# Optimization experiments

Measured on AMD Instinct MI355X. Metric: run time of the kernel, lower is better.

## Reference

```python
import jax, jax.numpy as jnp
import numpy as np

N = 1048576            # batch of query points
D = 3                  # n_in
N_LEVELS = 16
F_PER_LEVEL = 2
LOG2_T = 19
T = 1 << LOG2_T        # hash table size per level
MIN_RES = 16
MAX_RES = 512

# instant-NGP spatial hash primes (first prime = 1)
_PRIMES = np.array([1, 2654435761, 805459861], dtype=np.uint32)
# 2^D corner offsets of the interpolation cell, [8, D]
_OFFSETS = np.stack(np.meshgrid(*([np.arange(2)] * D), indexing='ij'), -1).reshape(-1, D).astype(np.float32)


def _resolutions():
    # geometric progression of grid resolutions between min and max
    b = np.exp((np.log(MAX_RES) - np.log(MIN_RES)) / (N_LEVELS - 1))
    return np.floor(MIN_RES * b ** np.arange(N_LEVELS)).astype(np.float32)


def setup_inputs() -> dict:
    key = jax.random.key(0)
    k1, k2 = jax.random.split(key)
    inp = jax.random.uniform(k1, (N, D), dtype=jnp.float32)  # inside bbox [0,1]^3
    params = jax.random.normal(k2, (N_LEVELS, T, F_PER_LEVEL), dtype=jnp.float32)
    return {"input": inp, "parameters": params}


def _hash_corners(ci):
    # ci: int32 [n, 8, D] integer grid coords -> int32 [n, 8] table index
    c = ci.astype(jnp.uint32)
    h = c[..., 0] * jnp.uint32(int(_PRIMES[0]))
    for d in range(1, D):
        h = h ^ (c[..., d] * jnp.uint32(int(_PRIMES[d])))
    return (h % jnp.uint32(T)).astype(jnp.int32)


def _encode(inp, parameters):
    # bbox min = 0, size = 1 -> normalized coords are the inputs themselves
    u = jnp.clip(inp, 0.0, 1.0)                       # [N, D]
    offs = jnp.asarray(_OFFSETS)                      # [8, D]
    offs_i = offs.astype(jnp.int32)
    res = jnp.asarray(_resolutions())                 # [L]

    def level(carry, xs):
        table_l, r = xs                               # [T, F], scalar
        pos = u * r                                   # [N, D]
        f = jnp.floor(pos)
        w = pos - f                                   # fractional part [N, D]
        ci = f.astype(jnp.int32)[:, None, :] + offs_i[None]   # [N, 8, D]
        idx = _hash_corners(ci)                       # [N, 8]
        feats = table_l[idx]                          # gather -> [N, 8, F]
        # multilinear interpolation weights: prod_d (w_d or 1-w_d)
        wts = jnp.prod(jnp.where(offs[None] > 0, w[:, None, :], 1.0 - w[:, None, :]), axis=-1)  # [N, 8]
        out_l = jnp.einsum('ncf,nc->nf', feats, wts)  # [N, F]
        return carry, out_l

    _, outs = jax.lax.scan(level, None, (parameters, res))    # [L, N, F]
    # combination_mode = "concat": [N, L*F]
    return jnp.transpose(outs, (1, 0, 2)).reshape(u.shape[0], N_LEVELS * F_PER_LEVEL)


def reference(input, parameters):
    return _encode(input, parameters)
```

## Files before the change

kernel.cpp:

```cpp
#include <hip/hip_runtime.h>
#include <cmath>
#include <cstdint>


constexpr uint32_t kLog2T = 19;
constexpr uint32_t kMask  = (1u << kLog2T) - 1u;
constexpr uint32_t kP1    = 2654435761u;
constexpr uint32_t kP2    = 805459861u;
constexpr uint32_t kN     = 1u << 20;
constexpr uint32_t kL     = 16;

typedef float v2f __attribute__((ext_vector_type(2)));
typedef float v4f __attribute__((ext_vector_type(4)));
typedef uint32_t v4u __attribute__((ext_vector_type(4)));

__device__ __forceinline__ v2f sel_half(v4f q, uint32_t hi) {
    v2f lo; lo.x = q.x; lo.y = q.y;
    v2f h2; h2.x = q.z; h2.y = q.w;
    return hi ? h2 : lo;
}

template <bool DIRECT>
__global__ __launch_bounds__(256) void ngp_encode_lm_kernel(
    const float* __restrict__ inp,
    const v4f* __restrict__ tbl4,
    v2f* __restrict__ dst,
    unsigned long long pk0, unsigned long long pk1,
    unsigned long long pk2, unsigned long long pk3)
{
    const uint32_t b = blockIdx.x;
    const uint32_t l = b >> 12;
    const uint32_t n = ((b & 4095u) << 8) + threadIdx.x;

    unsigned long long pk = (l < 8u) ? ((l < 4u) ? pk0 : pk1)
                                     : ((l < 12u) ? pk2 : pk3);
    const float r = (float)((uint32_t)(pk >> ((l & 3u) * 16u)) & 0xFFFFu);

    float x = __builtin_nontemporal_load(inp + n * 3u + 0u);
    float y = __builtin_nontemporal_load(inp + n * 3u + 1u);
    float z = __builtin_nontemporal_load(inp + n * 3u + 2u);
    x = fminf(fmaxf(x, 0.0f), 1.0f);
    y = fminf(fmaxf(y, 0.0f), 1.0f);
    z = fminf(fmaxf(z, 0.0f), 1.0f);

    const float px = x * r, py = y * r, pz = z * r;
    const float fx = floorf(px), fy = floorf(py), fz = floorf(pz);
    const float wx = px - fx, wy = py - fy, wz = pz - fz;

    const uint32_t xi  = (uint32_t)(int)fx;
    const uint32_t xi1 = xi + 1u;
    const uint32_t yi  = (uint32_t)(int)fy;
    const uint32_t zi  = (uint32_t)(int)fz;

    const uint32_t hy0 = yi * kP1, hy1 = hy0 + kP1;
    const uint32_t hz0 = zi * kP2, hz1 = hz0 + kP2;
    const uint32_t hyz00 = hy0 ^ hz0, hyz01 = hy0 ^ hz1;
    const uint32_t hyz10 = hy1 ^ hz0, hyz11 = hy1 ^ hz1;

    const uint32_t i000 = (xi  ^ hyz00) & kMask, i100 = (xi1 ^ hyz00) & kMask;
    const uint32_t i001 = (xi  ^ hyz01) & kMask, i101 = (xi1 ^ hyz01) & kMask;
    const uint32_t i010 = (xi  ^ hyz10) & kMask, i110 = (xi1 ^ hyz10) & kMask;
    const uint32_t i011 = (xi  ^ hyz11) & kMask, i111 = (xi1 ^ hyz11) & kMask;

    const uint64_t ba = (uint64_t)((const char*)tbl4 + ((size_t)l << 22));
    v4u srd;
    srd.x = (uint32_t)ba;
    srd.y = (uint32_t)(ba >> 32);
    srd.z = 0xFFFFFFFFu;
    srd.w = 0x00020000u;

    const uint32_t o00 = (i000 & ~1u) << 3, o01 = (i001 & ~1u) << 3;
    const uint32_t o10 = (i010 & ~1u) << 3, o11 = (i011 & ~1u) << 3;

    v4f q00, q01, q10, q11;
    asm volatile(
        "buffer_load_dwordx4 %0, %4, %8, 0 offen sc0\n\t"
        "buffer_load_dwordx4 %1, %5, %8, 0 offen sc0\n\t"
        "buffer_load_dwordx4 %2, %6, %8, 0 offen sc0\n\t"
        "buffer_load_dwordx4 %3, %7, %8, 0 offen sc0\n\t"
        "s_waitcnt vmcnt(0)"
        : "=&v"(q00), "=&v"(q01), "=&v"(q10), "=&v"(q11)
        : "v"(o00), "v"(o01), "v"(o10), "v"(o11), "s"(srd));

    v2f f000 = sel_half(q00, i000 & 1u), f100 = sel_half(q00, (i000 & 1u) ^ 1u);
    v2f f001 = sel_half(q01, i001 & 1u), f101 = sel_half(q01, (i001 & 1u) ^ 1u);
    v2f f010 = sel_half(q10, i010 & 1u), f110 = sel_half(q10, (i010 & 1u) ^ 1u);
    v2f f011 = sel_half(q11, i011 & 1u), f111 = sel_half(q11, (i011 & 1u) ^ 1u);

    if (xi & 1u) {
        const uint32_t p00 = i100 << 3, p01 = i101 << 3;
        const uint32_t p10 = i110 << 3, p11 = i111 << 3;
        v2f g00, g01, g10, g11;
        asm volatile(
            "buffer_load_dwordx2 %0, %4, %8, 0 offen sc0\n\t"
            "buffer_load_dwordx2 %1, %5, %8, 0 offen sc0\n\t"
            "buffer_load_dwordx2 %2, %6, %8, 0 offen sc0\n\t"
            "buffer_load_dwordx2 %3, %7, %8, 0 offen sc0\n\t"
            "s_waitcnt vmcnt(0)"
            : "=&v"(g00), "=&v"(g01), "=&v"(g10), "=&v"(g11)
            : "v"(p00), "v"(p01), "v"(p10), "v"(p11), "s"(srd));
        f100 = g00; f101 = g01; f110 = g10; f111 = g11;
    }

    const float wx1w = wx, wx0w = 1.0f - wx;
    const float wy1w = wy, wy0w = 1.0f - wy;
    const float wz1w = wz, wz0w = 1.0f - wz;
    const float wyz00w = wy0w * wz0w, wyz01w = wy0w * wz1w;
    const float wyz10w = wy1w * wz0w, wyz11w = wy1w * wz1w;

    float acc0 = 0.0f, acc1 = 0.0f;
#define NGP_ACC(F, W)                         \
    acc0 = fmaf((W), (F).x, acc0);            \
    acc1 = fmaf((W), (F).y, acc1);
    NGP_ACC(f000, wx0w * wyz00w) NGP_ACC(f100, wx1w * wyz00w)
    NGP_ACC(f001, wx0w * wyz01w) NGP_ACC(f101, wx1w * wyz01w)
    NGP_ACC(f010, wx0w * wyz10w) NGP_ACC(f110, wx1w * wyz10w)
    NGP_ACC(f011, wx0w * wyz11w) NGP_ACC(f111, wx1w * wyz11w)
#undef NGP_ACC

    v2f res; res.x = acc0; res.y = acc1;
    if (DIRECT) {
        __builtin_nontemporal_store(res, dst + (n * kL + l));
    } else {
        __builtin_nontemporal_store(res, dst + (l * kN + n));
    }
}

__global__ __launch_bounds__(256) void ngp_transpose_kernel(
    const v4f* __restrict__ ws4,
    v4f* __restrict__ out4)
{
    __shared__ v4f tile4[kL][65];
    const uint32_t t  = threadIdx.x;
    const uint32_t n0 = blockIdx.x * 128u;

    #pragma unroll
    for (uint32_t it = 0; it < 4; ++it) {
        const uint32_t l  = it * 4u + (t >> 6);
        const uint32_t pc = t & 63u;
        tile4[l][pc] = __builtin_nontemporal_load(ws4 + l * (kN / 2u) + (n0 >> 1) + pc);
    }
    __syncthreads();

    const v2f* tv = (const v2f*)&tile4[0][0];
    #pragma unroll
    for (uint32_t it = 0; it < 4; ++it) {
        const uint32_t p  = it * 32u + (t >> 3);
        const uint32_t lp = t & 7u;
        const v2f a = tv[(2u * lp + 0u) * 130u + p];
        const v2f b = tv[(2u * lp + 1u) * 130u + p];
        v4f o; o.x = a.x; o.y = a.y; o.z = b.x; o.w = b.y;
        __builtin_nontemporal_store(o, out4 + (n0 + p) * 8u + lp);
    }
}

extern "C" void kernel_launch(void* const* d_in, const int* in_sizes, int n_in,
                              void* d_out, int out_size, void* d_ws, size_t ws_size,
                              hipStream_t stream)
{
    const float* inp = (const float*)d_in[0];
    const v4f* tbl4  = (const v4f*)d_in[1];

    double b = std::exp((std::log(512.0) - std::log(16.0)) / 15.0);
    unsigned long long pk[4] = {0ull, 0ull, 0ull, 0ull};
    for (int k = 0; k < 16; ++k) {
        double v;
        if (k == 0)      v = 1.0;
        else if (k == 1) v = b;
        else if (k == 2) v = b * b;
        else             v = std::pow(b, (double)k);
        unsigned long long ri = (unsigned long long)std::floor(16.0 * v);
        pk[k >> 2] |= (ri & 0xFFFFull) << ((k & 3) * 16);
    }

    const uint32_t nblocks = (kN * kL) / 256u;
    const bool have_ws = ws_size >= (size_t)kN * kL * sizeof(v2f);

    if (have_ws) {
        hipLaunchKernelGGL((ngp_encode_lm_kernel<false>), dim3(nblocks), dim3(256), 0, stream,
                           inp, tbl4, (v2f*)d_ws, pk[0], pk[1], pk[2], pk[3]);
        hipLaunchKernelGGL(ngp_transpose_kernel, dim3(kN / 128u), dim3(256), 0, stream,
                           (const v4f*)d_ws, (v4f*)d_out);
    } else {
        hipLaunchKernelGGL((ngp_encode_lm_kernel<true>), dim3(nblocks), dim3(256), 0, stream,
                           inp, tbl4, (v2f*)d_out, pk[0], pk[1], pk[2], pk[3]);
    }
}
```

Measured before the change: 622.7 us.

## Spatially sort query points by coarse cell before hash-grid encoding

Adds a histogram, prefix-scan and scatter pass that buckets input points into a 16^3 coarse grid, so neighbouring points are encoded together. The goal is better cache locality for hash-table gathers at coarse levels. Encoding is split into two halves of eight levels, each followed by a transpose that scatters results back to the original point order. The cost is extra passes over the inputs, atomics, a 16 MB sorted buffer, and scattered output writes.

```diff
diff --git a/kernel.cpp b/kernel.cpp
--- a/kernel.cpp
+++ b/kernel.cpp
@@ -9,6 +9,7 @@
 constexpr uint32_t kP2    = 805459861u;
 constexpr uint32_t kN     = 1u << 20;
 constexpr uint32_t kL     = 16;
+constexpr uint32_t kBins  = 4096;
 
 typedef float v2f __attribute__((ext_vector_type(2)));
 typedef float v4f __attribute__((ext_vector_type(4)));
@@ -20,30 +21,86 @@
     return hi ? h2 : lo;
 }
 
-template <bool DIRECT>
-__global__ __launch_bounds__(256) void ngp_encode_lm_kernel(
-    const float* __restrict__ inp,
+__device__ __forceinline__ uint32_t cell_key(float x, float y, float z) {
+    uint32_t qx = (uint32_t)(x * 16.0f); qx = qx > 15u ? 15u : qx;
+    uint32_t qy = (uint32_t)(y * 16.0f); qy = qy > 15u ? 15u : qy;
+    uint32_t qz = (uint32_t)(z * 16.0f); qz = qz > 15u ? 15u : qz;
+    return (qz << 8) | (qy << 4) | qx;
+}
+
+
+__global__ __launch_bounds__(1024) void ngp_hist_kernel(
+    const float* __restrict__ inp, uint32_t* __restrict__ bins)
+{
+    __shared__ uint32_t h[kBins];
+    const uint32_t t = threadIdx.x;
+    for (uint32_t i = t; i < kBins; i += 1024u) h[i] = 0u;
+    __syncthreads();
+    const uint32_t base = blockIdx.x * 1024u * 16u;
+    #pragma unroll 4
+    for (uint32_t k = 0; k < 16u; ++k) {
+        const uint32_t n = base + k * 1024u + t;
+        float x = fminf(fmaxf(inp[n * 3u + 0u], 0.0f), 1.0f);
+        float y = fminf(fmaxf(inp[n * 3u + 1u], 0.0f), 1.0f);
+        float z = fminf(fmaxf(inp[n * 3u + 2u], 0.0f), 1.0f);
+        atomicAdd(&h[cell_key(x, y, z)], 1u);
+    }
+    __syncthreads();
+    for (uint32_t i = t; i < kBins; i += 1024u)
+        if (h[i]) atomicAdd(&bins[i], h[i]);
+}
+
+__global__ __launch_bounds__(64) void ngp_scan_kernel(
+    const uint32_t* __restrict__ bins, uint32_t* __restrict__ cursor)
+{
+    const uint32_t t = threadIdx.x;
+    uint32_t s = 0u;
+    for (uint32_t i = 0; i < 64u; ++i) s += bins[t * 64u + i];
+    uint32_t pre = s;
+    for (int d = 1; d < 64; d <<= 1) {
+        uint32_t u = __shfl_up(pre, d);
+        if ((int)t >= d) pre += u;
+    }
+    pre -= s;
+    for (uint32_t i = 0; i < 64u; ++i) {
+        cursor[t * 64u + i] = pre;
+        pre += bins[t * 64u + i];
+    }
+}
+
+__global__ __launch_bounds__(256) void ngp_scatter_kernel(
+    const float* __restrict__ inp, uint32_t* __restrict__ cursor,
+    v4f* __restrict__ sorted)
+{
+    const uint32_t n = blockIdx.x * 256u + threadIdx.x;
+    float x = fminf(fmaxf(inp[n * 3u + 0u], 0.0f), 1.0f);
+    float y = fminf(fmaxf(inp[n * 3u + 1u], 0.0f), 1.0f);
+    float z = fminf(fmaxf(inp[n * 3u + 2u], 0.0f), 1.0f);
+    const uint32_t key = cell_key(x, y, z);
+    const uint32_t pos = atomicAdd(&cursor[key], 1u);
+    v4f s; s.x = x; s.y = y; s.z = z; s.w = __uint_as_float(n);
+    sorted[pos] = s;
+}
+
+
+template <uint32_t BASE>
+__global__ __launch_bounds__(256) void ngp_encode_sorted_kernel(
+    const v4f* __restrict__ sorted,
     const v4f* __restrict__ tbl4,
-    v2f* __restrict__ dst,
+    v2f* __restrict__ wsres,
     unsigned long long pk0, unsigned long long pk1,
     unsigned long long pk2, unsigned long long pk3)
 {
     const uint32_t b = blockIdx.x;
-    const uint32_t l = b >> 12;
-    const uint32_t n = ((b & 4095u) << 8) + threadIdx.x;
+    const uint32_t l = BASE + (b >> 12);
+    const uint32_t j = ((b & 4095u) << 8) + threadIdx.x;
 
     unsigned long long pk = (l < 8u) ? ((l < 4u) ? pk0 : pk1)
                                      : ((l < 12u) ? pk2 : pk3);
     const float r = (float)((uint32_t)(pk >> ((l & 3u) * 16u)) & 0xFFFFu);
 
-    float x = __builtin_nontemporal_load(inp + n * 3u + 0u);
-    float y = __builtin_nontemporal_load(inp + n * 3u + 1u);
-    float z = __builtin_nontemporal_load(inp + n * 3u + 2u);
-    x = fminf(fmaxf(x, 0.0f), 1.0f);
-    y = fminf(fmaxf(y, 0.0f), 1.0f);
-    z = fminf(fmaxf(z, 0.0f), 1.0f);
-
-    const float px = x * r, py = y * r, pz = z * r;
+    const v4f s = sorted[j];
+    const float px = s.x * r, py = s.y * r, pz = s.z * r;
     const float fx = floorf(px), fy = floorf(py), fz = floorf(pz);
     const float wx = px - fx, wy = py - fy, wz = pz - fz;
 
@@ -119,39 +176,79 @@
 #undef NGP_ACC
 
     v2f res; res.x = acc0; res.y = acc1;
-    if (DIRECT) {
-        __builtin_nontemporal_store(res, dst + (n * kL + l));
-    } else {
-        __builtin_nontemporal_store(res, dst + (l * kN + n));
-    }
-}
-
-__global__ __launch_bounds__(256) void ngp_transpose_kernel(
+    __builtin_nontemporal_store(res, wsres + (l - BASE) * kN + j);
+}
+
+template <uint32_t BASE>
+__global__ __launch_bounds__(256) void ngp_untrans_kernel(
     const v4f* __restrict__ ws4,
+    const v4f* __restrict__ sorted,
     v4f* __restrict__ out4)
 {
-    __shared__ v4f tile4[kL][65];
+    __shared__ v4f tile4[8][65];
     const uint32_t t  = threadIdx.x;
-    const uint32_t n0 = blockIdx.x * 128u;
+    const uint32_t j0 = blockIdx.x * 128u;
 
     #pragma unroll
-    for (uint32_t it = 0; it < 4; ++it) {
-        const uint32_t l  = it * 4u + (t >> 6);
+    for (uint32_t it = 0; it < 2; ++it) {
+        const uint32_t lo = it * 4u + (t >> 6);
         const uint32_t pc = t & 63u;
-        tile4[l][pc] = __builtin_nontemporal_load(ws4 + l * (kN / 2u) + (n0 >> 1) + pc);
+        tile4[lo][pc] = ws4[lo * (kN / 2u) + (j0 >> 1) + pc];
     }
     __syncthreads();
 
     const v2f* tv = (const v2f*)&tile4[0][0];
     #pragma unroll
-    for (uint32_t it = 0; it < 4; ++it) {
-        const uint32_t p  = it * 32u + (t >> 3);
-        const uint32_t lp = t & 7u;
+    for (uint32_t it = 0; it < 2; ++it) {
+        const uint32_t p  = it * 64u + (t >> 2);
+        const uint32_t lp = t & 3u;
         const v2f a = tv[(2u * lp + 0u) * 130u + p];
         const v2f b = tv[(2u * lp + 1u) * 130u + p];
         v4f o; o.x = a.x; o.y = a.y; o.z = b.x; o.w = b.y;
-        __builtin_nontemporal_store(o, out4 + (n0 + p) * 8u + lp);
-    }
+        const uint32_t orig = __float_as_uint(sorted[j0 + p].w);
+        __builtin_nontemporal_store(o, out4 + orig * 8u + (BASE / 2u) + lp);
+    }
+}
+
+
+__global__ __launch_bounds__(256) void ngp_encode_direct_kernel(
+    const float* __restrict__ inp, const v4f* __restrict__ tbl4,
+    v2f* __restrict__ dst,
+    unsigned long long pk0, unsigned long long pk1,
+    unsigned long long pk2, unsigned long long pk3)
+{
+    const uint32_t b = blockIdx.x;
+    const uint32_t l = b >> 12;
+    const uint32_t n = ((b & 4095u) << 8) + threadIdx.x;
+    unsigned long long pk = (l < 8u) ? ((l < 4u) ? pk0 : pk1)
+                                     : ((l < 12u) ? pk2 : pk3);
+    const float r = (float)((uint32_t)(pk >> ((l & 3u) * 16u)) & 0xFFFFu);
+    float x = fminf(fmaxf(inp[n * 3u + 0u], 0.0f), 1.0f);
+    float y = fminf(fmaxf(inp[n * 3u + 1u], 0.0f), 1.0f);
+    float z = fminf(fmaxf(inp[n * 3u + 2u], 0.0f), 1.0f);
+    const float px = x * r, py = y * r, pz = z * r;
+    const float fx = floorf(px), fy = floorf(py), fz = floorf(pz);
+    const float wx = px - fx, wy = py - fy, wz = pz - fz;
+    const uint32_t xi = (uint32_t)(int)fx, yi = (uint32_t)(int)fy, zi = (uint32_t)(int)fz;
+    const uint32_t hy0 = yi * kP1, hy1 = hy0 + kP1;
+    const uint32_t hz0 = zi * kP2, hz1 = hz0 + kP2;
+    const v2f* tbl2 = (const v2f*)tbl4;
+    const uint32_t lb2 = l << kLog2T;
+    float acc0 = 0.0f, acc1 = 0.0f;
+#define NGP_C(HX, HY, HZ, W)                                        \
+    {                                                               \
+        uint32_t h = ((HX) ^ (HY) ^ (HZ)) & kMask;                  \
+        v2f f = tbl2[lb2 + h];                                      \
+        acc0 = fmaf((W), f.x, acc0); acc1 = fmaf((W), f.y, acc1);   \
+    }
+    const float wxa = 1.0f - wx, wya = 1.0f - wy, wza = 1.0f - wz;
+    NGP_C(xi,      hy0, hz0, wxa * wya * wza) NGP_C(xi + 1u, hy0, hz0, wx * wya * wza)
+    NGP_C(xi,      hy0, hz1, wxa * wya * wz ) NGP_C(xi + 1u, hy0, hz1, wx * wya * wz )
+    NGP_C(xi,      hy1, hz0, wxa * wy  * wza) NGP_C(xi + 1u, hy1, hz0, wx * wy  * wza)
+    NGP_C(xi,      hy1, hz1, wxa * wy  * wz ) NGP_C(xi + 1u, hy1, hz1, wx * wy  * wz )
+#undef NGP_C
+    v2f res; res.x = acc0; res.y = acc1;
+    dst[n * kL + l] = res;
 }
 
 extern "C" void kernel_launch(void* const* d_in, const int* in_sizes, int n_in,
@@ -173,16 +270,35 @@
         pk[k >> 2] |= (ri & 0xFFFFull) << ((k & 3) * 16);
     }
 
-    const uint32_t nblocks = (kN * kL) / 256u;
-    const bool have_ws = ws_size >= (size_t)kN * kL * sizeof(v2f);
-
-    if (have_ws) {
-        hipLaunchKernelGGL((ngp_encode_lm_kernel<false>), dim3(nblocks), dim3(256), 0, stream,
-                           inp, tbl4, (v2f*)d_ws, pk[0], pk[1], pk[2], pk[3]);
-        hipLaunchKernelGGL(ngp_transpose_kernel, dim3(kN / 128u), dim3(256), 0, stream,
-                           (const v4f*)d_ws, (v4f*)d_out);
+    const size_t offSorted = 0;
+    const size_t offBins   = (size_t)16 * 1024 * 1024;
+    const size_t offCursor = offBins + kBins * sizeof(uint32_t);
+    const size_t offRes    = offBins + 65536;
+    const size_t need      = offRes + (size_t)8 * kN * sizeof(v2f);
+
+    if (ws_size >= need) {
+        char* w = (char*)d_ws;
+        v4f*      sorted = (v4f*)(w + offSorted);
+        uint32_t* bins   = (uint32_t*)(w + offBins);
+        uint32_t* cursor = (uint32_t*)(w + offCursor);
+        v2f*      wsres  = (v2f*)(w + offRes);
+
+        hipMemsetAsync(bins, 0, kBins * sizeof(uint32_t), stream);
+        hipLaunchKernelGGL(ngp_hist_kernel, dim3(64), dim3(1024), 0, stream, inp, bins);
+        hipLaunchKernelGGL(ngp_scan_kernel, dim3(1), dim3(64), 0, stream, bins, cursor);
+        hipLaunchKernelGGL(ngp_scatter_kernel, dim3(kN / 256u), dim3(256), 0, stream,
+                           inp, cursor, sorted);
+
+        hipLaunchKernelGGL((ngp_encode_sorted_kernel<0>), dim3(32768), dim3(256), 0, stream,
+                           sorted, tbl4, wsres, pk[0], pk[1], pk[2], pk[3]);
+        hipLaunchKernelGGL((ngp_untrans_kernel<0>), dim3(kN / 128u), dim3(256), 0, stream,
+                           (const v4f*)wsres, sorted, (v4f*)d_out);
+        hipLaunchKernelGGL((ngp_encode_sorted_kernel<8>), dim3(32768), dim3(256), 0, stream,
+                           sorted, tbl4, wsres, pk[0], pk[1], pk[2], pk[3]);
+        hipLaunchKernelGGL((ngp_untrans_kernel<8>), dim3(kN / 128u), dim3(256), 0, stream,
+                           (const v4f*)wsres, sorted, (v4f*)d_out);
     } else {
-        hipLaunchKernelGGL((ngp_encode_lm_kernel<true>), dim3(nblocks), dim3(256), 0, stream,
+        hipLaunchKernelGGL(ngp_encode_direct_kernel, dim3((kN * kL) / 256u), dim3(256), 0, stream,
                            inp, tbl4, (v2f*)d_out, pk[0], pk[1], pk[2], pk[3]);
     }
 }
```

After: 555.3 us. 10.8% less time.
